# Optimization experiments

Hardware: AMD Instinct MI355X
Metric: run time of the kernel (lower is better)

## Reference

```python
import jax, jax.numpy as jnp
import numpy as np

N = 100000   # nodes
E = 1600000  # edges (before self loops)
D = 128      # input_dim
H1 = 128     # hidden_dim_1
H2 = 128     # hidden_dim_2
OUT = 1      # output_dim
G = 64       # number of graphs in the batch


def setup_inputs() -> dict:
    key = jax.random.key(0)
    ks = jax.random.split(key, 11)
    x = jax.random.normal(ks[0], (N, D), dtype=jnp.float32)
    edge_index = jax.random.randint(ks[1], (2, E), 0, N, dtype=jnp.int64)
    batch = jnp.sort(jax.random.randint(ks[2], (N,), 0, G, dtype=jnp.int64))
    s = 0.05
    W1 = jax.random.normal(ks[3], (D, H1), dtype=jnp.float32) * s
    b1 = jnp.zeros((H1,), dtype=jnp.float32)
    W2 = jax.random.normal(ks[4], (H1, H2), dtype=jnp.float32) * s
    b2 = jnp.zeros((H2,), dtype=jnp.float32)
    W_iou = jax.random.normal(ks[5], (H2, OUT), dtype=jnp.float32) * s
    b_iou = jnp.zeros((OUT,), dtype=jnp.float32)
    W_iop = jax.random.normal(ks[6], (H2, OUT), dtype=jnp.float32) * s
    b_iop = jnp.zeros((OUT,), dtype=jnp.float32)
    return dict(x=x, edge_index=edge_index, batch=batch,
                W1=W1, b1=b1, W2=W2, b2=b2,
                W_iou=W_iou, b_iou=b_iou, W_iop=W_iop, b_iop=b_iop)


def reference(x, edge_index, batch, W1, b1, W2, b2, W_iou, b_iou, W_iop, b_iop):
    n = x.shape[0]
    # add_self_loops
    loops = jnp.arange(n, dtype=edge_index.dtype)
    src = jnp.concatenate([edge_index[0], loops])
    dst = jnp.concatenate([edge_index[1], loops])
    # symmetric GCN normalization: deg over target nodes
    deg = jax.ops.segment_sum(jnp.ones_like(dst, dtype=x.dtype), dst, num_segments=n)
    dinv = jnp.where(deg > 0, jax.lax.rsqrt(deg), 0.0)
    norm = dinv[src] * dinv[dst]  # [E+N]

    def gcn_conv(h, W, b):
        hw = h @ W                                  # [N, H]
        m = hw[src] * norm[:, None]                 # gather + normalize [E+N, H]
        return jax.ops.segment_sum(m, dst, num_segments=n) + b  # scatter-add

    h = jax.nn.relu(gcn_conv(x, W1, b1))
    h = jax.nn.relu(gcn_conv(h, W2, b2))
    # global_max_pool over graph ids
    pooled = jax.ops.segment_max(h, batch, num_segments=G)
    pooled = jnp.where(jnp.isfinite(pooled), pooled, 0.0)  # guard empty graphs
    iou = pooled @ W_iou + b_iou
    iop = pooled @ W_iop + b_iop
    return jnp.concatenate([iou, iop], axis=1)  # [G, 2*OUT]
```

## Files before the change

### kernel.cpp

```cpp
#include <hip/hip_runtime.h>
#include <math.h>

typedef unsigned int u32;
typedef __attribute__((ext_vector_type(8))) short short8v;
typedef __attribute__((ext_vector_type(4))) float floatx4;

__device__ inline int rfl(int v) { return __builtin_amdgcn_readfirstlane(v); }

__device__ inline float blo(u32 u) { return __uint_as_float(u << 16); }
__device__ inline float bhi(u32 u) { return __uint_as_float(u & 0xffff0000u); }
__device__ inline u32 f2b(float f) {
    u32 u = __float_as_uint(f);
    return (u + 0x7fffu + ((u >> 16) & 1u)) >> 16;
}
__device__ inline u32 pack2(float a, float b) { return f2b(a) | (f2b(b) << 16); }

#define FILL_EPT 16
__global__ __launch_bounds__(256) void bfill_k(const int* __restrict__ src, const int* __restrict__ dst,
                                               u32* __restrict__ gcursor, u32* __restrict__ pairs,
                                               int E, int B, int CAP,
                                               const float* __restrict__ W1, const float* __restrict__ W2,
                                               ushort* __restrict__ W1t, ushort* __restrict__ W2t,
                                               u32* __restrict__ pooled) {
    __shared__ u32 lcnt[256];
    __shared__ u32 lbase[256];
    const int t = threadIdx.x;
    lcnt[t] = 0;
    __syncthreads();

    {
        const int b = blockIdx.x;
        if (b < 64) {
            int idx = b * 256 + t;
            int k = idx >> 7, jj = idx & 127;
            W1t[jj * 128 + k] = (ushort)f2b(W1[idx]);
            W2t[jj * 128 + k] = (ushort)f2b(W2[idx]);
        } else if (b < 96) {
            pooled[(b - 64) * 256 + t] = 0u;
        }
    }

    const int base_e = blockIdx.x * (256 * FILL_EPT);
    u32 pk[FILL_EPT];
    u32 bk[FILL_EPT];
    u32 rk[FILL_EPT];
#pragma unroll
    for (int q = 0; q < FILL_EPT / 4; ++q) {
        int e0 = base_e + (q * 256 + t) * 4;
        if (e0 + 3 < E) {
            int4 s4 = *(const int4*)(src + e0);
            int4 d4 = *(const int4*)(dst + e0);
            int ss[4] = {s4.x, s4.y, s4.z, s4.w};
            int dd[4] = {d4.x, d4.y, d4.z, d4.w};
#pragma unroll
            for (int r = 0; r < 4; ++r) {
                int j = q * 4 + r;
                u32 b = (u32)dd[r] >> 9;
                pk[j] = (u32)ss[r] | (((u32)dd[r] & 511u) << 17);
                bk[j] = b;
                rk[j] = atomicAdd(&lcnt[b], 1u);
            }
        } else {
#pragma unroll
            for (int r = 0; r < 4; ++r) {
                int j = q * 4 + r;
                int e = e0 + r;
                pk[j] = 0xFFFFFFFFu;
                if (e < E) {
                    int d = dst[e];
                    u32 b = (u32)d >> 9;
                    pk[j] = (u32)src[e] | (((u32)d & 511u) << 17);
                    bk[j] = b;
                    rk[j] = atomicAdd(&lcnt[b], 1u);
                }
            }
        }
    }
    __syncthreads();
    if (t < B) {
        u32 v = lcnt[t];
        lbase[t] = v ? atomicAdd(&gcursor[t], v) : 0u;
    }
    __syncthreads();
#pragma unroll
    for (int j = 0; j < FILL_EPT; ++j) {
        if (pk[j] != 0xFFFFFFFFu) {
            u32 b = bk[j];
            u32 pos = lbase[b] + rk[j];
            if (pos < (u32)CAP) pairs[(size_t)b * CAP + pos] = pk[j];
        }
    }
}

__device__ inline int swz(int row, int kbyte) { return row * 256 + (kbyte ^ ((row & 7) << 4)); }

template <bool BF16IN, bool SCALE>
__device__ __forceinline__ void gemm_body(const void* __restrict__ inp, const ushort* __restrict__ Wt,
                                          const float* __restrict__ dinv, ushort* __restrict__ outp,
                                          int N, int brow, char* Wl, int t) {
    {
        const uint4* g = (const uint4*)Wt;
#pragma unroll
        for (int i = 0; i < 4; ++i) {
            int f = t + i * 512;
            int r = f >> 4, kb = (f & 15) << 4;
            *(uint4*)(Wl + swz(r, kb)) = g[f];
        }
    }

    const int lane = t & 63;
    const int wave = t >> 6;
    const int l15 = lane & 15;
    const int g4 = lane >> 4;

    short8v a[2][4];
#pragma unroll
    for (int mt = 0; mt < 2; ++mt) {
        int row = brow + wave * 32 + mt * 16 + l15;
        bool ok = row < N;
        int rowc = ok ? row : 0;
#pragma unroll
        for (int ks = 0; ks < 4; ++ks) {
            uint4 v = make_uint4(0u, 0u, 0u, 0u);
            if (BF16IN) {
                if (ok) v = *(const uint4*)((const char*)inp + (size_t)rowc * 256 + (ks * 64 + g4 * 16));
            } else {
                if (ok) {
                    const float4* p = (const float4*)((const char*)inp + (size_t)rowc * 512 + (ks * 128 + g4 * 32));
                    float4 x0 = p[0], x1 = p[1];
                    v = make_uint4(pack2(x0.x, x0.y), pack2(x0.z, x0.w), pack2(x1.x, x1.y), pack2(x1.z, x1.w));
                }
            }
            a[mt][ks] = *(short8v*)&v;
        }
    }
    __syncthreads();

    floatx4 acc[2][8];
#pragma unroll
    for (int mt = 0; mt < 2; ++mt)
#pragma unroll
        for (int nt = 0; nt < 8; ++nt) acc[mt][nt] = (floatx4){0.f, 0.f, 0.f, 0.f};

#pragma unroll
    for (int ks = 0; ks < 4; ++ks) {
        int kb = ks * 64 + g4 * 16;
        short8v b[8];
#pragma unroll
        for (int nt = 0; nt < 8; ++nt)
            b[nt] = *(const short8v*)(Wl + swz(nt * 16 + l15, kb));
#pragma unroll
        for (int mt = 0; mt < 2; ++mt)
#pragma unroll
            for (int nt = 0; nt < 8; ++nt)
                acc[mt][nt] = __builtin_amdgcn_mfma_f32_16x16x32_bf16(a[mt][ks], b[nt], acc[mt][nt], 0, 0, 0);
    }

    const int r0w = g4 * 4;
#pragma unroll
    for (int mt = 0; mt < 2; ++mt) {
#pragma unroll
        for (int reg = 0; reg < 4; ++reg) {
            int grow = brow + wave * 32 + mt * 16 + r0w + reg;
            if (grow < N) {
                float sc = SCALE ? dinv[grow] : 1.f;
#pragma unroll
                for (int nt = 0; nt < 8; ++nt)
                    outp[grow * 128 + nt * 16 + l15] = (ushort)f2b(acc[mt][nt][reg] * sc);
            }
        }
    }
}

__global__ __launch_bounds__(512) void csort_gemm_k(const u32* __restrict__ pairs, const u32* __restrict__ gcursor,
                                                    u32* __restrict__ csr, uint2* __restrict__ rowinfo,
                                                    float* __restrict__ dinv, int N, int CAP, int B,
                                                    const float* __restrict__ x, const ushort* __restrict__ W1t,
                                                    ushort* __restrict__ hw1) {
    __shared__ __align__(16) char smem[32768];
    const int t = threadIdx.x;

    if (blockIdx.x >= B) {
        gemm_body<false, false>((const void*)x, W1t, nullptr, hw1, N, (blockIdx.x - B) * 256, smem, t);
        return;
    }

    u32* hist = (u32*)smem;
    u32* scanb = (u32*)(smem + 2048);
    const int b = blockIdx.x;
    const u32 base = (u32)b * (u32)CAP;
    u32 cnt = gcursor[b];
    if (cnt > (u32)CAP) cnt = (u32)CAP;

    hist[t] = 0u;
    __syncthreads();
    for (u32 j = t; j < cnt; j += 512) {
        u32 p = pairs[base + j];
        atomicAdd(&hist[p >> 17], 1u);
    }
    __syncthreads();
    u32 v = hist[t];
    scanb[t] = v;
    __syncthreads();
    for (int off = 1; off < 512; off <<= 1) {
        u32 x2 = (t >= off) ? scanb[t - off] : 0u;
        __syncthreads();
        scanb[t] += x2;
        __syncthreads();
    }
    u32 excl_t = scanb[t] - v;

    int i = (b << 9) + t;
    if (i < N) {
        rowinfo[i] = make_uint2(base + excl_t, v);
        dinv[i] = rsqrtf((float)(v + 1u));
    }
    __syncthreads();
    hist[t] = excl_t;
    __syncthreads();
    for (u32 j = t; j < cnt; j += 512) {
        u32 p = pairs[base + j];
        u32 loc = p >> 17;
        u32 pos = atomicAdd(&hist[loc], 1u);
        csr[base + pos] = p & 0x1FFFFu;
    }
}

__global__ __launch_bounds__(512) void gemm_mfma_k(const void* __restrict__ inp, const ushort* __restrict__ Wt,
                                                   const float* __restrict__ dinv,
                                                   ushort* __restrict__ outp, int N) {
    __shared__ __align__(16) char Wl[32768];
    gemm_body<true, true>(inp, Wt, dinv, outp, N, blockIdx.x * 256, Wl, threadIdx.x);
}

template <bool SCALE>
__device__ __forceinline__ void edge_row_accum8(const u32* __restrict__ hw, const u32* __restrict__ csr,
                                                const float* __restrict__ dinv,
                                                int r0, int deg, int lane, float& a0, float& a1) {
    int j = 0;
    for (; j + 8 <= deg; j += 8) {
        int s0 = rfl((int)csr[r0 + j + 0]);
        int s1 = rfl((int)csr[r0 + j + 1]);
        int s2 = rfl((int)csr[r0 + j + 2]);
        int s3 = rfl((int)csr[r0 + j + 3]);
        int s4 = rfl((int)csr[r0 + j + 4]);
        int s5 = rfl((int)csr[r0 + j + 5]);
        int s6 = rfl((int)csr[r0 + j + 6]);
        int s7 = rfl((int)csr[r0 + j + 7]);
        float w0 = SCALE ? dinv[s0] : 1.f;
        float w1 = SCALE ? dinv[s1] : 1.f;
        float w2 = SCALE ? dinv[s2] : 1.f;
        float w3 = SCALE ? dinv[s3] : 1.f;
        float w4 = SCALE ? dinv[s4] : 1.f;
        float w5 = SCALE ? dinv[s5] : 1.f;
        float w6 = SCALE ? dinv[s6] : 1.f;
        float w7 = SCALE ? dinv[s7] : 1.f;
        u32 u0 = hw[(size_t)s0 * 64 + lane];
        u32 u1 = hw[(size_t)s1 * 64 + lane];
        u32 u2 = hw[(size_t)s2 * 64 + lane];
        u32 u3 = hw[(size_t)s3 * 64 + lane];
        u32 u4 = hw[(size_t)s4 * 64 + lane];
        u32 u5 = hw[(size_t)s5 * 64 + lane];
        u32 u6 = hw[(size_t)s6 * 64 + lane];
        u32 u7 = hw[(size_t)s7 * 64 + lane];
        if (SCALE) {
            a0 = fmaf(w0, blo(u0), a0); a1 = fmaf(w0, bhi(u0), a1);
            a0 = fmaf(w1, blo(u1), a0); a1 = fmaf(w1, bhi(u1), a1);
            a0 = fmaf(w2, blo(u2), a0); a1 = fmaf(w2, bhi(u2), a1);
            a0 = fmaf(w3, blo(u3), a0); a1 = fmaf(w3, bhi(u3), a1);
            a0 = fmaf(w4, blo(u4), a0); a1 = fmaf(w4, bhi(u4), a1);
            a0 = fmaf(w5, blo(u5), a0); a1 = fmaf(w5, bhi(u5), a1);
            a0 = fmaf(w6, blo(u6), a0); a1 = fmaf(w6, bhi(u6), a1);
            a0 = fmaf(w7, blo(u7), a0); a1 = fmaf(w7, bhi(u7), a1);
        } else {
            a0 += blo(u0); a1 += bhi(u0);
            a0 += blo(u1); a1 += bhi(u1);
            a0 += blo(u2); a1 += bhi(u2);
            a0 += blo(u3); a1 += bhi(u3);
            a0 += blo(u4); a1 += bhi(u4);
            a0 += blo(u5); a1 += bhi(u5);
            a0 += blo(u6); a1 += bhi(u6);
            a0 += blo(u7); a1 += bhi(u7);
        }
    }
    if (j < deg) {
        const int rem = deg - j;
#pragma unroll
        for (int k = 0; k < 8; ++k) {
            int off = (k < rem) ? k : (rem - 1);
            int s = rfl((int)csr[r0 + j + off]);
            u32 u = hw[(size_t)s * 64 + lane];
            float w = SCALE ? dinv[s] : 1.f;
            bool valid = k < rem;
            float v0 = valid ? w * blo(u) : 0.f;
            float v1 = valid ? w * bhi(u) : 0.f;
            a0 += v0; a1 += v1;
        }
    }
}

__global__ __launch_bounds__(256) void edge_accum_k(const u32* __restrict__ hw, const uint2* __restrict__ rowinfo,
                                                    const u32* __restrict__ csr, const float* __restrict__ dinv,
                                                    const float* __restrict__ bias, u32* __restrict__ hout, int N) {
    const int lane = threadIdx.x & 63;
    const int wid = (blockIdx.x * blockDim.x + threadIdx.x) >> 6;
    const int nw = (gridDim.x * blockDim.x) >> 6;
    const float2 bb = ((const float2*)bias)[lane];

    for (int i = wid; i < N; i += nw) {
        uint2 ri = rowinfo[i];
        const int r0 = rfl((int)ri.x);
        const int deg = rfl((int)ri.y);
        float di = dinv[i];
        u32 us = hw[(size_t)i * 64 + lane];
        float a0 = di * blo(us), a1 = di * bhi(us);

        edge_row_accum8<true>(hw, csr, dinv, r0, deg, lane, a0, a1);

        a0 = fmaxf(fmaf(a0, di, bb.x), 0.f);
        a1 = fmaxf(fmaf(a1, di, bb.y), 0.f);
        hout[(size_t)i * 64 + lane] = pack2(a0, a1);
    }
}

__global__ __launch_bounds__(256) void edge_pool_k(const u32* __restrict__ hw, const uint2* __restrict__ rowinfo,
                                                   const u32* __restrict__ csr, const float* __restrict__ dinv,
                                                   const float* __restrict__ bias, const int* __restrict__ batch,
                                                   u32* __restrict__ pooled, int N, int chunk) {
    const int lane = threadIdx.x & 63;
    const int gwid = (blockIdx.x * blockDim.x + threadIdx.x) >> 6;
    const float2 bb = ((const float2*)bias)[lane];

    int i0 = gwid * chunk, i1 = min(N, i0 + chunk);
    float m0 = 0.f, m1 = 0.f;
    int gcur = -1;
    for (int i = i0; i < i1; ++i) {
        uint2 ri = rowinfo[i];
        const int r0 = rfl((int)ri.x);
        const int deg = rfl((int)ri.y);
        float di = dinv[i];
        u32 us = hw[(size_t)i * 64 + lane];
        float a0 = blo(us), a1 = bhi(us);

        edge_row_accum8<false>(hw, csr, nullptr, r0, deg, lane, a0, a1);

        a0 = fmaxf(fmaf(a0, di, bb.x), 0.f);
        a1 = fmaxf(fmaf(a1, di, bb.y), 0.f);

        int g = batch[i];
        if (g != gcur) {
            if (gcur >= 0) {
                atomicMax(pooled + gcur * 128 + lane * 2,     __float_as_uint(m0));
                atomicMax(pooled + gcur * 128 + lane * 2 + 1, __float_as_uint(m1));
            }
            gcur = g;
            m0 = m1 = 0.f;
        }
        m0 = fmaxf(m0, a0);
        m1 = fmaxf(m1, a1);
    }
    if (gcur >= 0) {
        atomicMax(pooled + gcur * 128 + lane * 2,     __float_as_uint(m0));
        atomicMax(pooled + gcur * 128 + lane * 2 + 1, __float_as_uint(m1));
    }
}

__global__ void final_k(const float* __restrict__ pooled, const float* __restrict__ Wu, const float* __restrict__ bu,
                        const float* __restrict__ Wp, const float* __restrict__ bp, float* __restrict__ out) {
    int t = threadIdx.x;
    int g = t >> 1, c = t & 1;
    const float* w = c ? Wp : Wu;
    const float* pr = pooled + g * 128;
    float s = 0.f;
    for (int k = 0; k < 128; k += 4)
        s += pr[k] * w[k] + pr[k + 1] * w[k + 1] + pr[k + 2] * w[k + 2] + pr[k + 3] * w[k + 3];
    out[g * 2 + c] = s + (c ? bp[0] : bu[0]);
}

extern "C" void kernel_launch(void* const* d_in, const int* in_sizes, int n_in,
                              void* d_out, int out_size, void* d_ws, size_t ws_size,
                              hipStream_t stream) {
    const float* x     = (const float*)d_in[0];
    const int*   ei    = (const int*)d_in[1];
    const int*   batch = (const int*)d_in[2];
    const float* W1    = (const float*)d_in[3];
    const float* b1    = (const float*)d_in[4];
    const float* W2    = (const float*)d_in[5];
    const float* b2    = (const float*)d_in[6];
    const float* Wu    = (const float*)d_in[7];
    const float* bu    = (const float*)d_in[8];
    const float* Wp    = (const float*)d_in[9];
    const float* bp    = (const float*)d_in[10];
    float* out = (float*)d_out;

    const int N = in_sizes[2];
    const int E = in_sizes[1] / 2;
    const int* src = ei;
    const int* dst = ei + E;

    const int B = (N + 511) >> 9;
    int avg = E / B;
    int CAP = avg + 6 * (int)sqrt((double)avg) + 64;
    CAP = (CAP + 63) & ~63;

    char* ws = (char*)d_ws;
    size_t o = 0;
    auto alloc = [&](size_t bytes) { size_t r = o; o += (bytes + 255) & ~(size_t)255; return r; };
    u32*   gcursor = (u32*)(ws + alloc(1024));
    float* dinv    = (float*)(ws + alloc((size_t)N * 4));
    uint2* rowinfo = (uint2*)(ws + alloc((size_t)N * 8));
    u32*   csr     = (u32*)(ws + alloc((size_t)B * CAP * 4));
    ushort* hwA    = (ushort*)(ws + alloc((size_t)N * 128 * 2));
    ushort* hwB    = (ushort*)(ws + alloc((size_t)N * 128 * 2));
    u32*   pooled  = (u32*)(ws + alloc(64 * 128 * 4));
    ushort* W1t    = (ushort*)(ws + alloc(128 * 128 * 2));
    ushort* W2t    = (ushort*)(ws + alloc(128 * 128 * 2));
    u32*   pairs   = (u32*)hwB;
    (void)ws_size; (void)n_in;

    const int gFill = (E + 256 * FILL_EPT - 1) / (256 * FILL_EPT);
    const int gGemm = (N + 255) / 256;
    const int nWaves = 2048 * 4;
    const int chunk = (N + nWaves - 1) / nWaves;

    hipMemsetAsync(gcursor, 0, 1024, stream);
    bfill_k<<<gFill, 256, 0, stream>>>(src, dst, gcursor, pairs, E, B, CAP, W1, W2, W1t, W2t, pooled);
    csort_gemm_k<<<B + gGemm, 512, 0, stream>>>(pairs, gcursor, csr, rowinfo, dinv, N, CAP, B, x, W1t, hwA);

    edge_accum_k<<<2048, 256, 0, stream>>>((const u32*)hwA, rowinfo, csr, dinv, b1, (u32*)hwB, N);
    gemm_mfma_k<<<gGemm, 512, 0, stream>>>((const void*)hwB, W2t, dinv, hwA, N);
    edge_pool_k<<<2048, 256, 0, stream>>>((const u32*)hwA, rowinfo, csr, dinv, b2, batch, pooled, N, chunk);

    final_k<<<1, 128, 0, stream>>>((const float*)pooled, Wu, bu, Wp, bp, out);
}
```

Before: 200.5 us.

## Prescale first-layer GEMM output by source dinv to drop per-edge dinv gathers

Adds a per-node in-degree counter filled with global atomics in the bucket-fill kernel. The first-layer GEMM, which runs concurrently with the CSR sort, uses that count to scale each row of x@W1 by rsqrt(deg+1). This lets the first aggregation kernel drop its per-edge random dinv[src] loads and use plain adds. The cost is 1.6M extra global atomics in the fill kernel and a larger memset.

```diff
diff --git a/kernel.cpp b/kernel.cpp
--- a/kernel.cpp
+++ b/kernel.cpp
@@ -17,8 +17,8 @@
 
 #define FILL_EPT 16
 __global__ __launch_bounds__(256) void bfill_k(const int* __restrict__ src, const int* __restrict__ dst,
-                                               u32* __restrict__ gcursor, u32* __restrict__ pairs,
-                                               int E, int B, int CAP,
+                                               u32* __restrict__ gcursor, u32* __restrict__ cnt,
+                                               u32* __restrict__ pairs, int E, int B, int CAP,
                                                const float* __restrict__ W1, const float* __restrict__ W2,
                                                ushort* __restrict__ W1t, ushort* __restrict__ W2t,
                                                u32* __restrict__ pooled) {
@@ -59,6 +59,7 @@
                 pk[j] = (u32)ss[r] | (((u32)dd[r] & 511u) << 17);
                 bk[j] = b;
                 rk[j] = atomicAdd(&lcnt[b], 1u);
+                atomicAdd(&cnt[dd[r]], 1u);
             }
         } else {
 #pragma unroll
@@ -72,6 +73,7 @@
                     pk[j] = (u32)src[e] | (((u32)d & 511u) << 17);
                     bk[j] = b;
                     rk[j] = atomicAdd(&lcnt[b], 1u);
+                    atomicAdd(&cnt[d], 1u);
                 }
             }
         }
@@ -94,9 +96,10 @@
 
 __device__ inline int swz(int row, int kbyte) { return row * 256 + (kbyte ^ ((row & 7) << 4)); }
 
-template <bool BF16IN, bool SCALE>
+template <bool BF16IN, int SMODE>
 __device__ __forceinline__ void gemm_body(const void* __restrict__ inp, const ushort* __restrict__ Wt,
-                                          const float* __restrict__ dinv, ushort* __restrict__ outp,
+                                          const float* __restrict__ dinv, const u32* __restrict__ cnt,
+                                          ushort* __restrict__ outp,
                                           int N, int brow, char* Wl, int t) {
     {
         const uint4* g = (const uint4*)Wt;
@@ -163,7 +166,7 @@
         for (int reg = 0; reg < 4; ++reg) {
             int grow = brow + wave * 32 + mt * 16 + r0w + reg;
             if (grow < N) {
-                float sc = SCALE ? dinv[grow] : 1.f;
+                float sc = (SMODE == 1) ? dinv[grow] : rsqrtf((float)(cnt[grow] + 1u));
 #pragma unroll
                 for (int nt = 0; nt < 8; ++nt)
                     outp[grow * 128 + nt * 16 + l15] = (ushort)f2b(acc[mt][nt][reg] * sc);
@@ -174,14 +177,15 @@
 
 __global__ __launch_bounds__(512) void csort_gemm_k(const u32* __restrict__ pairs, const u32* __restrict__ gcursor,
                                                     u32* __restrict__ csr, uint2* __restrict__ rowinfo,
-                                                    float* __restrict__ dinv, int N, int CAP, int B,
+                                                    float* __restrict__ dinv, const u32* __restrict__ cnt,
+                                                    int N, int CAP, int B,
                                                     const float* __restrict__ x, const ushort* __restrict__ W1t,
                                                     ushort* __restrict__ hw1) {
     __shared__ __align__(16) char smem[32768];
     const int t = threadIdx.x;
 
     if (blockIdx.x >= B) {
-        gemm_body<false, false>((const void*)x, W1t, nullptr, hw1, N, (blockIdx.x - B) * 256, smem, t);
+        gemm_body<false, 2>((const void*)x, W1t, nullptr, cnt, hw1, N, (blockIdx.x - B) * 256, smem, t);
         return;
     }
 
@@ -189,12 +193,12 @@
     u32* scanb = (u32*)(smem + 2048);
     const int b = blockIdx.x;
     const u32 base = (u32)b * (u32)CAP;
-    u32 cnt = gcursor[b];
-    if (cnt > (u32)CAP) cnt = (u32)CAP;
+    u32 c = gcursor[b];
+    if (c > (u32)CAP) c = (u32)CAP;
 
     hist[t] = 0u;
     __syncthreads();
-    for (u32 j = t; j < cnt; j += 512) {
+    for (u32 j = t; j < c; j += 512) {
         u32 p = pairs[base + j];
         atomicAdd(&hist[p >> 17], 1u);
     }
@@ -218,7 +222,7 @@
     __syncthreads();
     hist[t] = excl_t;
     __syncthreads();
-    for (u32 j = t; j < cnt; j += 512) {
+    for (u32 j = t; j < c; j += 512) {
         u32 p = pairs[base + j];
         u32 loc = p >> 17;
         u32 pos = atomicAdd(&hist[loc], 1u);
@@ -230,12 +234,10 @@
                                                    const float* __restrict__ dinv,
                                                    ushort* __restrict__ outp, int N) {
     __shared__ __align__(16) char Wl[32768];
-    gemm_body<true, true>(inp, Wt, dinv, outp, N, blockIdx.x * 256, Wl, threadIdx.x);
-}
-
-template <bool SCALE>
+    gemm_body<true, 1>(inp, Wt, dinv, nullptr, outp, N, blockIdx.x * 256, Wl, threadIdx.x);
+}
+
 __device__ __forceinline__ void edge_row_accum8(const u32* __restrict__ hw, const u32* __restrict__ csr,
-                                                const float* __restrict__ dinv,
                                                 int r0, int deg, int lane, float& a0, float& a1) {
     int j = 0;
     for (; j + 8 <= deg; j += 8) {
@@ -247,14 +249,6 @@
         int s5 = rfl((int)csr[r0 + j + 5]);
         int s6 = rfl((int)csr[r0 + j + 6]);
         int s7 = rfl((int)csr[r0 + j + 7]);
-        float w0 = SCALE ? dinv[s0] : 1.f;
-        float w1 = SCALE ? dinv[s1] : 1.f;
-        float w2 = SCALE ? dinv[s2] : 1.f;
-        float w3 = SCALE ? dinv[s3] : 1.f;
-        float w4 = SCALE ? dinv[s4] : 1.f;
-        float w5 = SCALE ? dinv[s5] : 1.f;
-        float w6 = SCALE ? dinv[s6] : 1.f;
-        float w7 = SCALE ? dinv[s7] : 1.f;
         u32 u0 = hw[(size_t)s0 * 64 + lane];
         u32 u1 = hw[(size_t)s1 * 64 + lane];
         u32 u2 = hw[(size_t)s2 * 64 + lane];
@@ -263,25 +257,14 @@
         u32 u5 = hw[(size_t)s5 * 64 + lane];
         u32 u6 = hw[(size_t)s6 * 64 + lane];
         u32 u7 = hw[(size_t)s7 * 64 + lane];
-        if (SCALE) {
-            a0 = fmaf(w0, blo(u0), a0); a1 = fmaf(w0, bhi(u0), a1);
-            a0 = fmaf(w1, blo(u1), a0); a1 = fmaf(w1, bhi(u1), a1);
-            a0 = fmaf(w2, blo(u2), a0); a1 = fmaf(w2, bhi(u2), a1);
-            a0 = fmaf(w3, blo(u3), a0); a1 = fmaf(w3, bhi(u3), a1);
-            a0 = fmaf(w4, blo(u4), a0); a1 = fmaf(w4, bhi(u4), a1);
-            a0 = fmaf(w5, blo(u5), a0); a1 = fmaf(w5, bhi(u5), a1);
-            a0 = fmaf(w6, blo(u6), a0); a1 = fmaf(w6, bhi(u6), a1);
-            a0 = fmaf(w7, blo(u7), a0); a1 = fmaf(w7, bhi(u7), a1);
-        } else {
-            a0 += blo(u0); a1 += bhi(u0);
-            a0 += blo(u1); a1 += bhi(u1);
-            a0 += blo(u2); a1 += bhi(u2);
-            a0 += blo(u3); a1 += bhi(u3);
-            a0 += blo(u4); a1 += bhi(u4);
-            a0 += blo(u5); a1 += bhi(u5);
-            a0 += blo(u6); a1 += bhi(u6);
-            a0 += blo(u7); a1 += bhi(u7);
-        }
+        a0 += blo(u0); a1 += bhi(u0);
+        a0 += blo(u1); a1 += bhi(u1);
+        a0 += blo(u2); a1 += bhi(u2);
+        a0 += blo(u3); a1 += bhi(u3);
+        a0 += blo(u4); a1 += bhi(u4);
+        a0 += blo(u5); a1 += bhi(u5);
+        a0 += blo(u6); a1 += bhi(u6);
+        a0 += blo(u7); a1 += bhi(u7);
     }
     if (j < deg) {
         const int rem = deg - j;
@@ -290,10 +273,8 @@
             int off = (k < rem) ? k : (rem - 1);
             int s = rfl((int)csr[r0 + j + off]);
             u32 u = hw[(size_t)s * 64 + lane];
-            float w = SCALE ? dinv[s] : 1.f;
-            bool valid = k < rem;
-            float v0 = valid ? w * blo(u) : 0.f;
-            float v1 = valid ? w * bhi(u) : 0.f;
+            float v0 = (k < rem) ? blo(u) : 0.f;
+            float v1 = (k < rem) ? bhi(u) : 0.f;
             a0 += v0; a1 += v1;
         }
     }
@@ -313,9 +294,9 @@
         const int deg = rfl((int)ri.y);
         float di = dinv[i];
         u32 us = hw[(size_t)i * 64 + lane];
-        float a0 = di * blo(us), a1 = di * bhi(us);
-
-        edge_row_accum8<true>(hw, csr, dinv, r0, deg, lane, a0, a1);
+        float a0 = blo(us), a1 = bhi(us);
+
+        edge_row_accum8(hw, csr, r0, deg, lane, a0, a1);
 
         a0 = fmaxf(fmaf(a0, di, bb.x), 0.f);
         a1 = fmaxf(fmaf(a1, di, bb.y), 0.f);
@@ -342,7 +323,7 @@
         u32 us = hw[(size_t)i * 64 + lane];
         float a0 = blo(us), a1 = bhi(us);
 
-        edge_row_accum8<false>(hw, csr, nullptr, r0, deg, lane, a0, a1);
+        edge_row_accum8(hw, csr, r0, deg, lane, a0, a1);
 
         a0 = fmaxf(fmaf(a0, di, bb.x), 0.f);
         a1 = fmaxf(fmaf(a1, di, bb.y), 0.f);
@@ -407,6 +388,7 @@
     size_t o = 0;
     auto alloc = [&](size_t bytes) { size_t r = o; o += (bytes + 255) & ~(size_t)255; return r; };
     u32*   gcursor = (u32*)(ws + alloc(1024));
+    u32*   cnt     = (u32*)(ws + alloc((size_t)N * 4));
     float* dinv    = (float*)(ws + alloc((size_t)N * 4));
     uint2* rowinfo = (uint2*)(ws + alloc((size_t)N * 8));
     u32*   csr     = (u32*)(ws + alloc((size_t)B * CAP * 4));
@@ -423,9 +405,9 @@
     const int nWaves = 2048 * 4;
     const int chunk = (N + nWaves - 1) / nWaves;
 
-    hipMemsetAsync(gcursor, 0, 1024, stream);
-    bfill_k<<<gFill, 256, 0, stream>>>(src, dst, gcursor, pairs, E, B, CAP, W1, W2, W1t, W2t, pooled);
-    csort_gemm_k<<<B + gGemm, 512, 0, stream>>>(pairs, gcursor, csr, rowinfo, dinv, N, CAP, B, x, W1t, hwA);
+    hipMemsetAsync(gcursor, 0, 1024 + ((size_t)N * 4 + 255 & ~(size_t)255), stream);
+    bfill_k<<<gFill, 256, 0, stream>>>(src, dst, gcursor, cnt, pairs, E, B, CAP, W1, W2, W1t, W2t, pooled);
+    csort_gemm_k<<<B + gGemm, 512, 0, stream>>>(pairs, gcursor, csr, rowinfo, dinv, cnt, N, CAP, B, x, W1t, hwA);
 
     edge_accum_k<<<2048, 256, 0, stream>>>((const u32*)hwA, rowinfo, csr, dinv, b1, (u32*)hwB, N);
     gemm_mfma_k<<<gGemm, 512, 0, stream>>>((const void*)hwB, W2t, dinv, hwA, N);
```

New measurement: 249.8 us. 24.6% more time.
